# Performance work log

Hardware: AMD Instinct MI355X
Metric: run time of the kernel (lower is better)

The kernel has to match this reference:

```python
import jax, jax.numpy as jnp
import numpy as np

N = 2048      # number of ROIs
C = 1024      # in_channels == inter_channels
G = 16        # groups
D = C // G    # per-group dim = 64


def _bbox_overlaps(b1, b2):
    # mmdet-1.x IoU with +1 pixel convention; b1:(N,4), b2:(M,4)
    area1 = (b1[:, 2] - b1[:, 0] + 1) * (b1[:, 3] - b1[:, 1] + 1)  # (N,)
    area2 = (b2[:, 2] - b2[:, 0] + 1) * (b2[:, 3] - b2[:, 1] + 1)  # (M,)
    lt = jnp.maximum(b1[:, None, :2], b2[None, :, :2])             # (N,M,2)
    rb = jnp.minimum(b1[:, None, 2:], b2[None, :, 2:])             # (N,M,2)
    wh = jnp.clip(rb - lt + 1, 0)
    inter = wh[..., 0] * wh[..., 1]                                # (N,M)
    return inter / (area1[:, None] + area2[None, :] - inter)


def setup_inputs() -> dict:
    key = jax.random.key(0)
    ks = jax.random.split(key, 9)
    in_x = jax.random.normal(ks[0], (N, C), dtype=jnp.float32)
    # valid boxes: [batch_idx, x1, y1, x2, y2]
    xy = jax.random.uniform(ks[1], (N, 2), minval=0.0, maxval=800.0)
    wh = jax.random.uniform(ks[2], (N, 2), minval=8.0, maxval=200.0)
    rois = jnp.concatenate([jnp.zeros((N, 1)), xy, xy + wh], axis=1).astype(jnp.float32)
    s = 1.0 / np.sqrt(C)
    W0 = jax.random.normal(ks[3], (C, C), dtype=jnp.float32) * s
    b0 = jnp.zeros((C,), dtype=jnp.float32)
    W1 = jax.random.normal(ks[4], (C, C), dtype=jnp.float32) * s
    b1 = jnp.zeros((C,), dtype=jnp.float32)
    # grouped 1x1 conv: per group maps C channels -> D channels
    Wout = jax.random.normal(ks[5], (G, D, C), dtype=jnp.float32) * s
    bout = jnp.zeros((C,), dtype=jnp.float32)
    return {"in_x": in_x, "rois": rois, "W0": W0, "b0": b0, "W1": W1,
            "b1": b1, "Wout": Wout, "bout": bout}


def reference(in_x, rois, W0, b0, W1, b1, Wout, bout):
    # self-attention path: in_ref_x = in_x, ref_rois = rois
    # embed convs are pre-activation (relu -> 1x1 conv), shared for x and ref_x
    def embed(v):
        v = jax.nn.relu(v) @ W0.T + b0
        v = jax.nn.relu(v) @ W1.T + b1
        return v
    x = embed(in_x)                      # (N, C)
    ref_x = x                            # shared convs, same input
    xg = x.reshape(N, G, D)
    rg = ref_x.reshape(N, G, D)
    scores = jnp.einsum('ngd,mgd->ngm', xg, rg) / jnp.sqrt(jnp.float32(D))  # (N,G,N)
    ious = _bbox_overlaps(rois[:, 1:], rois[:, 1:])                          # (N,N)
    scores = scores + jnp.log(ious[:, None, :] + 1e-6)
    attn = jax.nn.softmax(scores, axis=2)                                    # (N,G,N)
    y = jnp.einsum('ngm,mc->ngc', attn, in_x)                                # (N,G,C)
    out = jnp.einsum('ngc,goc->ngo', y, Wout).reshape(N, C) + bout           # (N,C)
    return out
```

## Files before the change

kernel.cpp:

```cpp
#include <hip/hip_runtime.h>
#include <math.h>

constexpr int NROI = 2048;
constexpr int CDIM = 1024;
constexpr int NG   = 16;
constexpr int DH   = 64;

typedef __attribute__((ext_vector_type(8))) short short8;
typedef __attribute__((ext_vector_type(4))) float floatx4;

#define MFMA_BF16(a, b, c) __builtin_amdgcn_mfma_f32_16x16x32_bf16((a), (b), (c), 0, 0, 0)

__device__ __forceinline__ short f2bf(float f) {
  unsigned u = __float_as_uint(f);
  unsigned r = 0x7fffu + ((u >> 16) & 1u);
  return (short)((u + r) >> 16);
}
__device__ __forceinline__ short f2bf_rtz(float f) {
  return (short)(__float_as_uint(f) >> 16);
}
__device__ __forceinline__ unsigned pack2(float a, float b) {
  return (unsigned)(unsigned short)f2bf(a) | ((unsigned)(unsigned short)f2bf(b) << 16);
}

typedef __attribute__((address_space(1))) void GV;
typedef __attribute__((address_space(3))) void LV;
__device__ __forceinline__ void gl2lds16(const void* g, void* l) {
  __builtin_amdgcn_global_load_lds((GV*)g, (LV*)l, 16, 0, 0);
}

__device__ __forceinline__ short8 brelu(short8 v) {
  union { short8 s; unsigned u[4]; } x; x.s = v;
#pragma unroll
  for (int i = 0; i < 4; ++i) {
    unsigned m = (x.u[i] >> 15) & 0x10001u;
    x.u[i] &= ~(m * 0xFFFFu);
  }
  return x.s;
}

__global__ __launch_bounds__(256) void conv_iou(
    const float* __restrict__ in_x, const float* __restrict__ W0,
    const float* __restrict__ W1, const float* __restrict__ Wout,
    const float* __restrict__ rois,
    short* __restrict__ xin_b, short* __restrict__ W0b,
    short* __restrict__ W1b, short* __restrict__ Woutb,
    unsigned short* __restrict__ biasln)
{
  const int b = blockIdx.x;
  if (b < 2048) {
    const int i = b * 256 + threadIdx.x;
    {
      const float4 v = ((const float4*)in_x)[i];
      uint2 u; u.x = pack2(v.x, v.y); u.y = pack2(v.z, v.w);
      ((uint2*)xin_b)[i] = u;
    }
    if (i < 262144) {
      float4 v = ((const float4*)W0)[i];
      uint2 u; u.x = pack2(v.x, v.y); u.y = pack2(v.z, v.w);
      ((uint2*)W0b)[i] = u;
      v = ((const float4*)W1)[i];
      u.x = pack2(v.x, v.y); u.y = pack2(v.z, v.w);
      ((uint2*)W1b)[i] = u;
      v = ((const float4*)Wout)[i];
      u.x = pack2(v.x, v.y); u.y = pack2(v.z, v.w);
      ((uint2*)Woutb)[i] = u;
    }
  } else {
    const int p = (b - 2048) * 256 + threadIdx.x;
    const int q = p >> 11, k = p & 2047;
    const float qx1 = rois[q * 5 + 1], qy1 = rois[q * 5 + 2];
    const float qx2 = rois[q * 5 + 3], qy2 = rois[q * 5 + 4];
    const float qa = (qx2 - qx1 + 1.f) * (qy2 - qy1 + 1.f);
    const float kx1 = rois[k * 5 + 1], ky1 = rois[k * 5 + 2];
    const float kx2 = rois[k * 5 + 3], ky2 = rois[k * 5 + 4];
    const float ka = (kx2 - kx1 + 1.f) * (ky2 - ky1 + 1.f);
    float iw = fminf(qx2, kx2) - fmaxf(qx1, kx1) + 1.f;
    float ih = fminf(qy2, ky2) - fmaxf(qy1, ky1) + 1.f;
    iw = fmaxf(iw, 0.f); ih = fmaxf(ih, 0.f);
    const float inter = iw * ih;
    const float iou = inter / (qa + ka - inter);
    biasln[p] = (unsigned short)f2bf(__logf(iou + 1e-6f));
  }
}

__global__ __launch_bounds__(256) void gemm128(
    const short* __restrict__ A, const short* __restrict__ BW0,
    const short* __restrict__ BWout, const float* __restrict__ b0,
    short* __restrict__ t0b, short* __restrict__ zT)
{
  __shared__ short As[16 * 512];
  __shared__ short Bs[16 * 512];
  const int t = threadIdx.x, w = t >> 6, lane = t & 63;
  const int wm = w >> 1, wn = w & 1;
  const int row0 = blockIdx.y * 128;
  const int col0g = blockIdx.x * 128;
  const int isW0 = col0g < 1024;
  const short* B = isW0 ? BW0 : BWout;
  const int col0 = col0g & 1023;
  const int srow = lane & 15, skq = (lane >> 4) * 8;

  floatx4 acc[4][4];
#pragma unroll
  for (int i = 0; i < 4; ++i)
#pragma unroll
    for (int j = 0; j < 4; ++j) acc[i][j] = (floatx4){0.f, 0.f, 0.f, 0.f};

  for (int k0 = 0; k0 < CDIM; k0 += 64) {
    __syncthreads();
#pragma unroll
    for (int q = 0; q < 4; ++q) {
      const int f = w * 4 + q, rt = f >> 1, kh = f & 1;
      gl2lds16(A + (size_t)(row0 + rt * 16 + srow) * CDIM + k0 + kh * 32 + skq,
               &As[f * 512]);
      gl2lds16(B + (size_t)(col0 + rt * 16 + srow) * CDIM + k0 + kh * 32 + skq,
               &Bs[f * 512]);
    }
    __syncthreads();
#pragma unroll
    for (int kh = 0; kh < 2; ++kh) {
      short8 a[4], bf[4];
#pragma unroll
      for (int i = 0; i < 4; ++i) {
        a[i] = *(const short8*)&As[(((wm * 4 + i) * 2) + kh) * 512 + lane * 8];
        if (isW0) a[i] = brelu(a[i]);
      }
#pragma unroll
      for (int j = 0; j < 4; ++j)
        bf[j] = *(const short8*)&Bs[(((wn * 4 + j) * 2) + kh) * 512 + lane * 8];
#pragma unroll
      for (int i = 0; i < 4; ++i)
#pragma unroll
        for (int j = 0; j < 4; ++j)
          acc[i][j] = MFMA_BF16(a[i], bf[j], acc[i][j]);
    }
  }

  const int colL = lane & 15, qq = lane >> 4;
  if (isW0) {
    float bj[4];
#pragma unroll
    for (int j = 0; j < 4; ++j) bj[j] = b0[col0 + wn * 64 + j * 16 + colL];
#pragma unroll
    for (int i = 0; i < 4; ++i)
#pragma unroll
      for (int j = 0; j < 4; ++j)
#pragma unroll
        for (int r = 0; r < 4; ++r) {
          const int row = row0 + wm * 64 + i * 16 + qq * 4 + r;
          const int cc  = col0 + wn * 64 + j * 16 + colL;
          t0b[(size_t)row * CDIM + cc] = f2bf(acc[i][j][r] + bj[j]);
        }
  } else {
#pragma unroll
    for (int i = 0; i < 4; ++i)
#pragma unroll
      for (int j = 0; j < 4; ++j) {
        unsigned long long u = 0;
#pragma unroll
        for (int r = 0; r < 4; ++r)
          u |= ((unsigned long long)(unsigned short)f2bf(acc[i][j][r])) << (16 * r);
        const int cc  = col0 + wn * 64 + j * 16 + colL;
        const int row = row0 + wm * 64 + i * 16 + qq * 4;
        *(unsigned long long*)&zT[(size_t)cc * NROI + row] = u;
      }
  }
}

__global__ __launch_bounds__(256) void gemm_relu_nt(
    const short* __restrict__ A, const short* __restrict__ B,
    const float* __restrict__ bias, short* __restrict__ C)
{
  __shared__ short As[8 * 512];
  __shared__ short Bs[8 * 512];
  const int t = threadIdx.x, w = t >> 6, lane = t & 63;
  const int wm = w >> 1, wn = w & 1;
  const int row0 = blockIdx.y * 64, col0 = blockIdx.x * 64;
  const int rlo = lane & 15, khi = (lane >> 4) * 8;

  floatx4 acc[2][2];
#pragma unroll
  for (int i = 0; i < 2; ++i)
#pragma unroll
    for (int j = 0; j < 2; ++j) acc[i][j] = (floatx4){0.f, 0.f, 0.f, 0.f};

  for (int k0 = 0; k0 < CDIM; k0 += 64) {
    __syncthreads();
#pragma unroll
    for (int kh = 0; kh < 2; ++kh) {
      gl2lds16(A + (size_t)(row0 + w * 16 + rlo) * CDIM + k0 + kh * 32 + khi,
               &As[(w * 2 + kh) * 512]);
      gl2lds16(B + (size_t)(col0 + w * 16 + rlo) * CDIM + k0 + kh * 32 + khi,
               &Bs[(w * 2 + kh) * 512]);
    }
    __syncthreads();
#pragma unroll
    for (int kh = 0; kh < 2; ++kh) {
      short8 a0 = *(const short8*)&As[((wm * 2 + 0) * 2 + kh) * 512 + lane * 8];
      short8 a1 = *(const short8*)&As[((wm * 2 + 1) * 2 + kh) * 512 + lane * 8];
      a0 = brelu(a0); a1 = brelu(a1);
      const short8 b0f = *(const short8*)&Bs[((wn * 2 + 0) * 2 + kh) * 512 + lane * 8];
      const short8 b1f = *(const short8*)&Bs[((wn * 2 + 1) * 2 + kh) * 512 + lane * 8];
      acc[0][0] = MFMA_BF16(a0, b0f, acc[0][0]);
      acc[0][1] = MFMA_BF16(a0, b1f, acc[0][1]);
      acc[1][0] = MFMA_BF16(a1, b0f, acc[1][0]);
      acc[1][1] = MFMA_BF16(a1, b1f, acc[1][1]);
    }
  }

  const int colL = lane & 15, qq = lane >> 4;
  float bj[2];
  bj[0] = bias[col0 + wn * 32 + colL];
  bj[1] = bias[col0 + wn * 32 + 16 + colL];
#pragma unroll
  for (int i = 0; i < 2; ++i)
#pragma unroll
    for (int j = 0; j < 2; ++j)
#pragma unroll
      for (int r = 0; r < 4; ++r) {
        const int row = row0 + wm * 32 + i * 16 + qq * 4 + r;
        const int cc  = col0 + wn * 32 + j * 16 + colL;
        C[(size_t)row * CDIM + cc] = f2bf(acc[i][j][r] + bj[j]);
      }
}

__global__ __launch_bounds__(512) void attn_ln(
    const short* __restrict__ Xb,
    const short* __restrict__ ZTb,
    const unsigned short* __restrict__ biasln,
    const float* __restrict__ bout,
    float* __restrict__ Out)
{
  const int g  = blockIdx.y;
  const int n0 = blockIdx.x * 128;
  const int t = threadIdx.x, w = t >> 6, lane = t & 63;
  const int col = lane & 15, qq = lane >> 4;
  const int t16 = (w >> 1) * 16, h32 = (w & 1) * 32;
  const int rlo = lane & 15, khi = (lane >> 4) * 8;

  __shared__ short Kf[2][8 * 512];
  __shared__ short Vf[2][8 * 512];
  __shared__ short Pf[8 * 1024];

  const size_t qoff = (size_t)(n0 + w * 16 + col) * CDIM + g * DH;
  const short8 qf0 = *(const short8*)(Xb + qoff + qq * 8);
  const short8 qf1 = *(const short8*)(Xb + qoff + 32 + qq * 8);

  floatx4 oc[4];
#pragma unroll
  for (int dt = 0; dt < 4; ++dt) oc[dt] = (floatx4){0.f, 0.f, 0.f, 0.f};
  float lsum[4] = {0.f, 0.f, 0.f, 0.f};

  const int qrow0 = n0 + w * 16 + qq * 4;

  uint2 bbc[4], bbn[4];
#pragma unroll
  for (int ct = 0; ct < 4; ++ct)
    bbc[ct] = *(const uint2*)(biasln + (size_t)(ct * 16 + col) * NROI + qrow0);

  gl2lds16(Xb + (size_t)(t16 + rlo) * CDIM + g * DH + h32 + khi, &Kf[0][w * 512]);
  gl2lds16(ZTb + (size_t)(g * DH + t16 + rlo) * NROI + h32 + khi, &Vf[0][w * 512]);
  __syncthreads();

  for (int it = 0; it < NROI / 64; ++it) {
    const int p = it & 1;
    const int m0 = it * 64;
    if (it + 1 < NROI / 64) {
      const int m1 = m0 + 64;
      gl2lds16(Xb + (size_t)(m1 + t16 + rlo) * CDIM + g * DH + h32 + khi,
               &Kf[1 - p][w * 512]);
      gl2lds16(ZTb + (size_t)(g * DH + t16 + rlo) * NROI + m1 + h32 + khi,
               &Vf[1 - p][w * 512]);
#pragma unroll
      for (int ct = 0; ct < 4; ++ct)
        bbn[ct] = *(const uint2*)(biasln + (size_t)(m1 + ct * 16 + col) * NROI + qrow0);
    }

    floatx4 sc[4];
#pragma unroll
    for (int ct = 0; ct < 4; ++ct) {
      const short8 b0 = *(const short8*)&Kf[p][(ct * 2 + 0) * 512 + lane * 8];
      const short8 b1 = *(const short8*)&Kf[p][(ct * 2 + 1) * 512 + lane * 8];
      floatx4 z4 = (floatx4){0.f, 0.f, 0.f, 0.f};
      z4 = MFMA_BF16(qf0, b0, z4);
      z4 = MFMA_BF16(qf1, b1, z4);
      sc[ct] = z4;
    }

#pragma unroll
    for (int ct = 0; ct < 4; ++ct) {
      const unsigned ux = bbc[ct].x, uy = bbc[ct].y;
      sc[ct][0] = __expf(fmaf(sc[ct][0], 0.125f, __uint_as_float(ux << 16)));
      sc[ct][1] = __expf(fmaf(sc[ct][1], 0.125f, __uint_as_float(ux & 0xFFFF0000u)));
      sc[ct][2] = __expf(fmaf(sc[ct][2], 0.125f, __uint_as_float(uy << 16)));
      sc[ct][3] = __expf(fmaf(sc[ct][3], 0.125f, __uint_as_float(uy & 0xFFFF0000u)));
    }
#pragma unroll
    for (int r = 0; r < 4; ++r)
      lsum[r] += sc[0][r] + sc[1][r] + sc[2][r] + sc[3][r];

    {
      short* pw = &Pf[w * 1024];
#pragma unroll
      for (int ct = 0; ct < 4; ++ct) {
        const int key = ct * 16 + col;
        const int base = (key >> 5) * 512 + (key & 7);
#pragma unroll
        for (int r = 0; r < 4; ++r) {
          const int dl = (4 * qq + r) + ((key >> 3) & 3) * 16;
          pw[base + dl * 8] = f2bf_rtz(sc[ct][r]);
        }
      }
      const short8 pa0 = *(const short8*)&pw[0 * 512 + lane * 8];
      const short8 pa1 = *(const short8*)&pw[1 * 512 + lane * 8];
#pragma unroll
      for (int dt = 0; dt < 4; ++dt) {
        const short8 v0 = *(const short8*)&Vf[p][(dt * 2 + 0) * 512 + lane * 8];
        const short8 v1 = *(const short8*)&Vf[p][(dt * 2 + 1) * 512 + lane * 8];
        oc[dt] = MFMA_BF16(pa0, v0, oc[dt]);
        oc[dt] = MFMA_BF16(pa1, v1, oc[dt]);
      }
    }
    __syncthreads();
#pragma unroll
    for (int ct = 0; ct < 4; ++ct) bbc[ct] = bbn[ct];
  }

#pragma unroll
  for (int r = 0; r < 4; ++r) {
    float s = lsum[r];
    s += __shfl_xor(s, 1); s += __shfl_xor(s, 2);
    s += __shfl_xor(s, 4); s += __shfl_xor(s, 8);
    lsum[r] = s;
  }
#pragma unroll
  for (int dt = 0; dt < 4; ++dt) {
    const float bo = bout[g * DH + dt * 16 + col];
#pragma unroll
    for (int r = 0; r < 4; ++r)
      Out[(size_t)(qrow0 + r) * CDIM + g * DH + dt * 16 + col] =
          oc[dt][r] / lsum[r] + bo;
  }
}

extern "C" void kernel_launch(void* const* d_in, const int* in_sizes, int n_in,
                              void* d_out, int out_size, void* d_ws, size_t ws_size,
                              hipStream_t stream) {
  const float* in_x = (const float*)d_in[0];
  const float* rois = (const float*)d_in[1];
  const float* W0   = (const float*)d_in[2];
  const float* b0   = (const float*)d_in[3];
  const float* W1   = (const float*)d_in[4];
  const float* b1   = (const float*)d_in[5];
  const float* Wout = (const float*)d_in[6];
  const float* bout = (const float*)d_in[7];
  char* w8 = (char*)d_ws;

  short* xin_b = (short*)w8;
  short* W0b   = (short*)(w8 + ((size_t)4 << 20));
  short* W1b   = (short*)(w8 + ((size_t)6 << 20));
  short* Woutb = (short*)(w8 + ((size_t)8 << 20));
  short* zT    = (short*)(w8 + ((size_t)10 << 20));
  unsigned short* biasln = (unsigned short*)(w8 + ((size_t)14 << 20));
  short* xb  = xin_b;
  short* t0b = (short*)d_out;

  conv_iou<<<2048 + 16384, 256, 0, stream>>>(in_x, W0, W1, Wout, rois,
                                             xin_b, W0b, W1b, Woutb, biasln);
  gemm128<<<dim3(16, 16), 256, 0, stream>>>(xin_b, W0b, Woutb, b0, t0b, zT);
  gemm_relu_nt<<<dim3(16, 32), 256, 0, stream>>>(t0b, W1b, b1, xb);
  attn_ln<<<dim3(NROI / 128, NG), 512, 0, stream>>>(xb, zT, biasln, bout,
                                                    (float*)d_out);
}
```

Baseline: 205.5 us.

## Rewrite GEMM and attention kernels as single-wave blocks with double-buffered LDS

Replaces the 4-wave GEMM kernels and the 8-wave attention kernel with one-wavefront-per-block kernels. They prefetch the next K/V or A/B tile into a second LDS buffer and use manual vmcnt waits and sched barriers in place of __syncthreads. The two embed GEMMs share one template. The attention kernel processes 32 queries per wave, writes packed P tiles to LDS with 64-bit stores, and normalises with a reciprocal. The aim is to remove block-level barriers and overlap loads with MFMA work. The cost is smaller tiles and possibly low occupancy, because each single wave holds a large LDS footprint. The last prefetch also reads past the end of each buffer.

```diff
diff --git a/kernel.cpp b/kernel.cpp
--- a/kernel.cpp
+++ b/kernel.cpp
@@ -16,11 +16,11 @@
   unsigned r = 0x7fffu + ((u >> 16) & 1u);
   return (short)((u + r) >> 16);
 }
-__device__ __forceinline__ short f2bf_rtz(float f) {
-  return (short)(__float_as_uint(f) >> 16);
-}
 __device__ __forceinline__ unsigned pack2(float a, float b) {
   return (unsigned)(unsigned short)f2bf(a) | ((unsigned)(unsigned short)f2bf(b) << 16);
+}
+__device__ __forceinline__ unsigned pack_rtz(float a, float b) {
+  return (__float_as_uint(a) >> 16) | (__float_as_uint(b) & 0xFFFF0000u);
 }
 
 typedef __attribute__((address_space(1))) void GV;
@@ -28,6 +28,10 @@
 __device__ __forceinline__ void gl2lds16(const void* g, void* l) {
   __builtin_amdgcn_global_load_lds((GV*)g, (LV*)l, 16, 0, 0);
 }
+
+__device__ __forceinline__ void waitcnt_vm16() { __builtin_amdgcn_s_waitcnt(0x4F70); }
+__device__ __forceinline__ void waitcnt_vm12() { __builtin_amdgcn_s_waitcnt(0x0F7C); }
+__device__ __forceinline__ void sbar() { __builtin_amdgcn_sched_barrier(0); }
 
 __device__ __forceinline__ short8 brelu(short8 v) {
   union { short8 s; unsigned u[4]; } x; x.s = v;
@@ -84,262 +88,238 @@
   }
 }
 
-__global__ __launch_bounds__(256) void gemm128(
-    const short* __restrict__ A, const short* __restrict__ BW0,
-    const short* __restrict__ BWout, const float* __restrict__ b0,
-    short* __restrict__ t0b, short* __restrict__ zT)
+template <int FUSED>
+__global__ __launch_bounds__(64) void gemm_wp(
+    const short* __restrict__ A, const short* __restrict__ Ba,
+    const short* __restrict__ Bb, const float* __restrict__ bias,
+    short* __restrict__ outRM, short* __restrict__ outTR)
 {
-  __shared__ short As[16 * 512];
-  __shared__ short Bs[16 * 512];
-  const int t = threadIdx.x, w = t >> 6, lane = t & 63;
-  const int wm = w >> 1, wn = w & 1;
-  const int row0 = blockIdx.y * 128;
-  const int col0g = blockIdx.x * 128;
-  const int isW0 = col0g < 1024;
-  const short* B = isW0 ? BW0 : BWout;
-  const int col0 = col0g & 1023;
-  const int srow = lane & 15, skq = (lane >> 4) * 8;
-
-  floatx4 acc[4][4];
+  const int lane = threadIdx.x;
+  const int c = lane & 15, Q = lane >> 4;
+  const int rlo = c, khi = Q * 8;
+  const int row0 = blockIdx.y * 64;
+  int colb; const short* B; bool doRelu, toTR;
+  if (FUSED) {
+    const int bx = blockIdx.x;
+    const bool isW0 = bx < 32;
+    colb = (bx & 31) * 32;
+    B = isW0 ? Ba : Bb;
+    doRelu = isW0; toTR = !isW0;
+  } else {
+    colb = blockIdx.x * 32; B = Ba; doRelu = true; toTR = false;
+  }
+
+  __shared__ short As[2][8 * 512];
+  __shared__ short Bs[2][4 * 512];
+
+  floatx4 acc[4][2];
 #pragma unroll
   for (int i = 0; i < 4; ++i)
 #pragma unroll
-    for (int j = 0; j < 4; ++j) acc[i][j] = (floatx4){0.f, 0.f, 0.f, 0.f};
-
-  for (int k0 = 0; k0 < CDIM; k0 += 64) {
-    __syncthreads();
-#pragma unroll
-    for (int q = 0; q < 4; ++q) {
-      const int f = w * 4 + q, rt = f >> 1, kh = f & 1;
-      gl2lds16(A + (size_t)(row0 + rt * 16 + srow) * CDIM + k0 + kh * 32 + skq,
-               &As[f * 512]);
-      gl2lds16(B + (size_t)(col0 + rt * 16 + srow) * CDIM + k0 + kh * 32 + skq,
-               &Bs[f * 512]);
-    }
-    __syncthreads();
-#pragma unroll
-    for (int kh = 0; kh < 2; ++kh) {
-      short8 a[4], bf[4];
-#pragma unroll
-      for (int i = 0; i < 4; ++i) {
-        a[i] = *(const short8*)&As[(((wm * 4 + i) * 2) + kh) * 512 + lane * 8];
-        if (isW0) a[i] = brelu(a[i]);
-      }
-#pragma unroll
-      for (int j = 0; j < 4; ++j)
-        bf[j] = *(const short8*)&Bs[(((wn * 4 + j) * 2) + kh) * 512 + lane * 8];
+    for (int j = 0; j < 2; ++j) acc[i][j] = (floatx4){0.f, 0.f, 0.f, 0.f};
+
+#pragma unroll
+  for (int f = 0; f < 8; ++f)
+    gl2lds16(A + (size_t)(row0 + (f >> 1) * 16 + rlo) * CDIM + (f & 1) * 32 + khi,
+             &As[0][f * 512]);
+#pragma unroll
+  for (int f = 0; f < 4; ++f)
+    gl2lds16(B + (size_t)(colb + (f >> 1) * 16 + rlo) * CDIM + (f & 1) * 32 + khi,
+             &Bs[0][f * 512]);
+
+  for (int it = 0; it < 16; ++it) {
+    const int p = it & 1;
+    const int k1 = (it + 1) * 64;
+    sbar();
+#pragma unroll
+    for (int f = 0; f < 8; ++f)
+      gl2lds16(A + (size_t)(row0 + (f >> 1) * 16 + rlo) * CDIM + k1 + (f & 1) * 32 + khi,
+               &As[1 - p][f * 512]);
+#pragma unroll
+    for (int f = 0; f < 4; ++f)
+      gl2lds16(B + (size_t)(colb + (f >> 1) * 16 + rlo) * CDIM + k1 + (f & 1) * 32 + khi,
+               &Bs[1 - p][f * 512]);
+    waitcnt_vm12();
+    sbar();
+
+    short8 af[8], bf[4];
+    if (doRelu) {
+#pragma unroll
+      for (int f = 0; f < 8; ++f)
+        af[f] = brelu(*(const short8*)&As[p][f * 512 + lane * 8]);
+    } else {
+#pragma unroll
+      for (int f = 0; f < 8; ++f)
+        af[f] = *(const short8*)&As[p][f * 512 + lane * 8];
+    }
+#pragma unroll
+    for (int f = 0; f < 4; ++f) bf[f] = *(const short8*)&Bs[p][f * 512 + lane * 8];
+#pragma unroll
+    for (int kh = 0; kh < 2; ++kh)
 #pragma unroll
       for (int i = 0; i < 4; ++i)
 #pragma unroll
-        for (int j = 0; j < 4; ++j)
-          acc[i][j] = MFMA_BF16(a[i], bf[j], acc[i][j]);
-    }
-  }
-
-  const int colL = lane & 15, qq = lane >> 4;
-  if (isW0) {
-    float bj[4];
-#pragma unroll
-    for (int j = 0; j < 4; ++j) bj[j] = b0[col0 + wn * 64 + j * 16 + colL];
+        for (int j = 0; j < 2; ++j)
+          acc[i][j] = MFMA_BF16(af[i * 2 + kh], bf[j * 2 + kh], acc[i][j]);
+  }
+
+  if (!toTR) {
+    const float bj0 = bias[colb + c];
+    const float bj1 = bias[colb + 16 + c];
 #pragma unroll
     for (int i = 0; i < 4; ++i)
 #pragma unroll
-      for (int j = 0; j < 4; ++j)
-#pragma unroll
-        for (int r = 0; r < 4; ++r) {
-          const int row = row0 + wm * 64 + i * 16 + qq * 4 + r;
-          const int cc  = col0 + wn * 64 + j * 16 + colL;
-          t0b[(size_t)row * CDIM + cc] = f2bf(acc[i][j][r] + bj[j]);
-        }
+      for (int r = 0; r < 4; ++r) {
+        const int row = row0 + i * 16 + Q * 4 + r;
+        outRM[(size_t)row * CDIM + colb + c]      = f2bf(acc[i][0][r] + bj0);
+        outRM[(size_t)row * CDIM + colb + 16 + c] = f2bf(acc[i][1][r] + bj1);
+      }
   } else {
 #pragma unroll
     for (int i = 0; i < 4; ++i)
 #pragma unroll
-      for (int j = 0; j < 4; ++j) {
-        unsigned long long u = 0;
-#pragma unroll
-        for (int r = 0; r < 4; ++r)
-          u |= ((unsigned long long)(unsigned short)f2bf(acc[i][j][r])) << (16 * r);
-        const int cc  = col0 + wn * 64 + j * 16 + colL;
-        const int row = row0 + wm * 64 + i * 16 + qq * 4;
-        *(unsigned long long*)&zT[(size_t)cc * NROI + row] = u;
-      }
-  }
-}
-
-__global__ __launch_bounds__(256) void gemm_relu_nt(
-    const short* __restrict__ A, const short* __restrict__ B,
-    const float* __restrict__ bias, short* __restrict__ C)
-{
-  __shared__ short As[8 * 512];
-  __shared__ short Bs[8 * 512];
-  const int t = threadIdx.x, w = t >> 6, lane = t & 63;
-  const int wm = w >> 1, wn = w & 1;
-  const int row0 = blockIdx.y * 64, col0 = blockIdx.x * 64;
-  const int rlo = lane & 15, khi = (lane >> 4) * 8;
-
-  floatx4 acc[2][2];
-#pragma unroll
-  for (int i = 0; i < 2; ++i)
-#pragma unroll
-    for (int j = 0; j < 2; ++j) acc[i][j] = (floatx4){0.f, 0.f, 0.f, 0.f};
-
-  for (int k0 = 0; k0 < CDIM; k0 += 64) {
-    __syncthreads();
-#pragma unroll
-    for (int kh = 0; kh < 2; ++kh) {
-      gl2lds16(A + (size_t)(row0 + w * 16 + rlo) * CDIM + k0 + kh * 32 + khi,
-               &As[(w * 2 + kh) * 512]);
-      gl2lds16(B + (size_t)(col0 + w * 16 + rlo) * CDIM + k0 + kh * 32 + khi,
-               &Bs[(w * 2 + kh) * 512]);
-    }
-    __syncthreads();
-#pragma unroll
-    for (int kh = 0; kh < 2; ++kh) {
-      short8 a0 = *(const short8*)&As[((wm * 2 + 0) * 2 + kh) * 512 + lane * 8];
-      short8 a1 = *(const short8*)&As[((wm * 2 + 1) * 2 + kh) * 512 + lane * 8];
-      a0 = brelu(a0); a1 = brelu(a1);
-      const short8 b0f = *(const short8*)&Bs[((wn * 2 + 0) * 2 + kh) * 512 + lane * 8];
-      const short8 b1f = *(const short8*)&Bs[((wn * 2 + 1) * 2 + kh) * 512 + lane * 8];
-      acc[0][0] = MFMA_BF16(a0, b0f, acc[0][0]);
-      acc[0][1] = MFMA_BF16(a0, b1f, acc[0][1]);
-      acc[1][0] = MFMA_BF16(a1, b0f, acc[1][0]);
-      acc[1][1] = MFMA_BF16(a1, b1f, acc[1][1]);
-    }
-  }
-
-  const int colL = lane & 15, qq = lane >> 4;
-  float bj[2];
-  bj[0] = bias[col0 + wn * 32 + colL];
-  bj[1] = bias[col0 + wn * 32 + 16 + colL];
-#pragma unroll
-  for (int i = 0; i < 2; ++i)
-#pragma unroll
-    for (int j = 0; j < 2; ++j)
-#pragma unroll
-      for (int r = 0; r < 4; ++r) {
-        const int row = row0 + wm * 32 + i * 16 + qq * 4 + r;
-        const int cc  = col0 + wn * 32 + j * 16 + colL;
-        C[(size_t)row * CDIM + cc] = f2bf(acc[i][j][r] + bj[j]);
-      }
-}
-
-__global__ __launch_bounds__(512) void attn_ln(
+      for (int j = 0; j < 2; ++j) {
+        unsigned long long u =
+            (unsigned long long)pack2(acc[i][j][0], acc[i][j][1]) |
+            ((unsigned long long)pack2(acc[i][j][2], acc[i][j][3]) << 32);
+        *(unsigned long long*)&outTR[(size_t)(colb + j * 16 + c) * NROI +
+                                     row0 + i * 16 + Q * 4] = u;
+      }
+  }
+}
+
+__global__ __launch_bounds__(64) void attn_wp(
     const short* __restrict__ Xb,
     const short* __restrict__ ZTb,
     const unsigned short* __restrict__ biasln,
     const float* __restrict__ bout,
     float* __restrict__ Out)
 {
-  const int g  = blockIdx.y;
-  const int n0 = blockIdx.x * 128;
-  const int t = threadIdx.x, w = t >> 6, lane = t & 63;
-  const int col = lane & 15, qq = lane >> 4;
-  const int t16 = (w >> 1) * 16, h32 = (w & 1) * 32;
-  const int rlo = lane & 15, khi = (lane >> 4) * 8;
-
-  __shared__ short Kf[2][8 * 512];
-  __shared__ short Vf[2][8 * 512];
-  __shared__ short Pf[8 * 1024];
-
-  const size_t qoff = (size_t)(n0 + w * 16 + col) * CDIM + g * DH;
-  const short8 qf0 = *(const short8*)(Xb + qoff + qq * 8);
-  const short8 qf1 = *(const short8*)(Xb + qoff + 32 + qq * 8);
-
-  floatx4 oc[4];
-#pragma unroll
-  for (int dt = 0; dt < 4; ++dt) oc[dt] = (floatx4){0.f, 0.f, 0.f, 0.f};
-  float lsum[4] = {0.f, 0.f, 0.f, 0.f};
-
-  const int qrow0 = n0 + w * 16 + qq * 4;
-
-  uint2 bbc[4], bbn[4];
-#pragma unroll
-  for (int ct = 0; ct < 4; ++ct)
-    bbc[ct] = *(const uint2*)(biasln + (size_t)(ct * 16 + col) * NROI + qrow0);
-
-  gl2lds16(Xb + (size_t)(t16 + rlo) * CDIM + g * DH + h32 + khi, &Kf[0][w * 512]);
-  gl2lds16(ZTb + (size_t)(g * DH + t16 + rlo) * NROI + h32 + khi, &Vf[0][w * 512]);
-  __syncthreads();
-
-  for (int it = 0; it < NROI / 64; ++it) {
+  const int g = blockIdx.y, q0 = blockIdx.x * 32;
+  const int lane = threadIdx.x;
+  const int c = lane & 15, Q = lane >> 4;
+  const int rlo = c, khi = Q * 8;
+  const int goff = g * DH;
+
+  __shared__ short KT[2][8 * 512];
+  __shared__ short VT[2][8 * 512];
+  __shared__ short PT[2][1024];
+
+  short8 qf[2][2];
+#pragma unroll
+  for (int s = 0; s < 2; ++s)
+#pragma unroll
+    for (int h = 0; h < 2; ++h)
+      qf[s][h] = *(const short8*)(Xb + (size_t)(q0 + s * 16 + c) * CDIM + goff +
+                                  h * 32 + Q * 8);
+
+  floatx4 oc[2][4];
+#pragma unroll
+  for (int s = 0; s < 2; ++s)
+#pragma unroll
+    for (int dt = 0; dt < 4; ++dt) oc[s][dt] = (floatx4){0.f, 0.f, 0.f, 0.f};
+  float ls[2] = {0.f, 0.f};
+
+#pragma unroll
+  for (int f = 0; f < 8; ++f) {
+    gl2lds16(Xb + (size_t)((f >> 1) * 16 + rlo) * CDIM + goff + (f & 1) * 32 + khi,
+             &KT[0][f * 512]);
+    gl2lds16(ZTb + (size_t)(goff + (f >> 1) * 16 + rlo) * NROI + (f & 1) * 32 + khi,
+             &VT[0][f * 512]);
+  }
+
+  for (int it = 0; it < 32; ++it) {
     const int p = it & 1;
-    const int m0 = it * 64;
-    if (it + 1 < NROI / 64) {
-      const int m1 = m0 + 64;
-      gl2lds16(Xb + (size_t)(m1 + t16 + rlo) * CDIM + g * DH + h32 + khi,
-               &Kf[1 - p][w * 512]);
-      gl2lds16(ZTb + (size_t)(g * DH + t16 + rlo) * NROI + m1 + h32 + khi,
-               &Vf[1 - p][w * 512]);
+    const int m0 = it * 64, m1 = m0 + 64;
+    sbar();
+#pragma unroll
+    for (int f = 0; f < 8; ++f) {
+      gl2lds16(Xb + (size_t)(m1 + (f >> 1) * 16 + rlo) * CDIM + goff + (f & 1) * 32 + khi,
+               &KT[1 - p][f * 512]);
+      gl2lds16(ZTb + (size_t)(goff + (f >> 1) * 16 + rlo) * NROI + m1 + (f & 1) * 32 + khi,
+               &VT[1 - p][f * 512]);
+    }
+    waitcnt_vm16();
+    sbar();
+
+    short8 kf[8];
+#pragma unroll
+    for (int f = 0; f < 8; ++f)
+      kf[f] = *(const short8*)&KT[p][f * 512 + lane * 8];
+
+    uint2 bb[2][4];
+#pragma unroll
+    for (int s = 0; s < 2; ++s)
 #pragma unroll
       for (int ct = 0; ct < 4; ++ct)
-        bbn[ct] = *(const uint2*)(biasln + (size_t)(m1 + ct * 16 + col) * NROI + qrow0);
-    }
-
-    floatx4 sc[4];
-#pragma unroll
-    for (int ct = 0; ct < 4; ++ct) {
-      const short8 b0 = *(const short8*)&Kf[p][(ct * 2 + 0) * 512 + lane * 8];
-      const short8 b1 = *(const short8*)&Kf[p][(ct * 2 + 1) * 512 + lane * 8];
-      floatx4 z4 = (floatx4){0.f, 0.f, 0.f, 0.f};
-      z4 = MFMA_BF16(qf0, b0, z4);
-      z4 = MFMA_BF16(qf1, b1, z4);
-      sc[ct] = z4;
-    }
-
-#pragma unroll
-    for (int ct = 0; ct < 4; ++ct) {
-      const unsigned ux = bbc[ct].x, uy = bbc[ct].y;
-      sc[ct][0] = __expf(fmaf(sc[ct][0], 0.125f, __uint_as_float(ux << 16)));
-      sc[ct][1] = __expf(fmaf(sc[ct][1], 0.125f, __uint_as_float(ux & 0xFFFF0000u)));
-      sc[ct][2] = __expf(fmaf(sc[ct][2], 0.125f, __uint_as_float(uy << 16)));
-      sc[ct][3] = __expf(fmaf(sc[ct][3], 0.125f, __uint_as_float(uy & 0xFFFF0000u)));
-    }
+        bb[s][ct] = *(const uint2*)(biasln + (size_t)(q0 + s * 16 + c) * NROI +
+                                    m0 + ct * 16 + Q * 4);
+
+#pragma unroll
+    for (int s = 0; s < 2; ++s) {
+      floatx4 sc[4];
+#pragma unroll
+      for (int ct = 0; ct < 4; ++ct) {
+        floatx4 z = (floatx4){0.f, 0.f, 0.f, 0.f};
+        z = MFMA_BF16(kf[ct * 2 + 0], qf[s][0], z);
+        z = MFMA_BF16(kf[ct * 2 + 1], qf[s][1], z);
+        sc[ct] = z;
+      }
+#pragma unroll
+      for (int ct = 0; ct < 4; ++ct) {
+        const unsigned ux = bb[s][ct].x, uy = bb[s][ct].y;
+        sc[ct][0] = __expf(fmaf(sc[ct][0], 0.125f, __uint_as_float(ux << 16)));
+        sc[ct][1] = __expf(fmaf(sc[ct][1], 0.125f, __uint_as_float(ux & 0xFFFF0000u)));
+        sc[ct][2] = __expf(fmaf(sc[ct][2], 0.125f, __uint_as_float(uy << 16)));
+        sc[ct][3] = __expf(fmaf(sc[ct][3], 0.125f, __uint_as_float(uy & 0xFFFF0000u)));
+        ls[s] += sc[ct][0] + sc[ct][1] + sc[ct][2] + sc[ct][3];
+        const int h  = (4 * ct + Q) >> 3;
+        const int o  = (2 * ct + (Q >> 1)) & 3;
+        const int j0 = (Q & 1) * 4;
+        const unsigned long long u =
+            (unsigned long long)pack_rtz(sc[ct][0], sc[ct][1]) |
+            ((unsigned long long)pack_rtz(sc[ct][2], sc[ct][3]) << 32);
+        *(unsigned long long*)&PT[s][h * 512 + (c + 16 * o) * 8 + j0] = u;
+      }
+    }
+
+    short8 vf[8];
+#pragma unroll
+    for (int f = 0; f < 8; ++f)
+      vf[f] = *(const short8*)&VT[p][f * 512 + lane * 8];
+#pragma unroll
+    for (int s = 0; s < 2; ++s) {
+      const short8 pa0 = *(const short8*)&PT[s][lane * 8];
+      const short8 pa1 = *(const short8*)&PT[s][512 + lane * 8];
+#pragma unroll
+      for (int dt = 0; dt < 4; ++dt) {
+        oc[s][dt] = MFMA_BF16(pa0, vf[dt * 2 + 0], oc[s][dt]);
+        oc[s][dt] = MFMA_BF16(pa1, vf[dt * 2 + 1], oc[s][dt]);
+      }
+    }
+  }
+
+#pragma unroll
+  for (int s = 0; s < 2; ++s) {
+    float v = ls[s];
+    v += __shfl_xor(v, 16);
+    v += __shfl_xor(v, 32);
+    ls[s] = v;
+  }
+#pragma unroll
+  for (int s = 0; s < 2; ++s) {
+    float inv[4];
 #pragma unroll
     for (int r = 0; r < 4; ++r)
-      lsum[r] += sc[0][r] + sc[1][r] + sc[2][r] + sc[3][r];
-
-    {
-      short* pw = &Pf[w * 1024];
-#pragma unroll
-      for (int ct = 0; ct < 4; ++ct) {
-        const int key = ct * 16 + col;
-        const int base = (key >> 5) * 512 + (key & 7);
-#pragma unroll
-        for (int r = 0; r < 4; ++r) {
-          const int dl = (4 * qq + r) + ((key >> 3) & 3) * 16;
-          pw[base + dl * 8] = f2bf_rtz(sc[ct][r]);
-        }
-      }
-      const short8 pa0 = *(const short8*)&pw[0 * 512 + lane * 8];
-      const short8 pa1 = *(const short8*)&pw[1 * 512 + lane * 8];
-#pragma unroll
-      for (int dt = 0; dt < 4; ++dt) {
-        const short8 v0 = *(const short8*)&Vf[p][(dt * 2 + 0) * 512 + lane * 8];
-        const short8 v1 = *(const short8*)&Vf[p][(dt * 2 + 1) * 512 + lane * 8];
-        oc[dt] = MFMA_BF16(pa0, v0, oc[dt]);
-        oc[dt] = MFMA_BF16(pa1, v1, oc[dt]);
-      }
-    }
-    __syncthreads();
-#pragma unroll
-    for (int ct = 0; ct < 4; ++ct) bbc[ct] = bbn[ct];
-  }
-
-#pragma unroll
-  for (int r = 0; r < 4; ++r) {
-    float s = lsum[r];
-    s += __shfl_xor(s, 1); s += __shfl_xor(s, 2);
-    s += __shfl_xor(s, 4); s += __shfl_xor(s, 8);
-    lsum[r] = s;
-  }
-#pragma unroll
-  for (int dt = 0; dt < 4; ++dt) {
-    const float bo = bout[g * DH + dt * 16 + col];
-#pragma unroll
-    for (int r = 0; r < 4; ++r)
-      Out[(size_t)(qrow0 + r) * CDIM + g * DH + dt * 16 + col] =
-          oc[dt][r] / lsum[r] + bo;
+      inv[r] = __builtin_amdgcn_rcpf(__shfl(ls[s], Q * 4 + r));
+#pragma unroll
+    for (int dt = 0; dt < 4; ++dt) {
+      const float bo = bout[goff + dt * 16 + c];
+#pragma unroll
+      for (int r = 0; r < 4; ++r)
+        Out[(size_t)(q0 + s * 16 + Q * 4 + r) * CDIM + goff + dt * 16 + c] =
+            oc[s][dt][r] * inv[r] + bo;
+    }
   }
 }
 
@@ -367,8 +347,8 @@
 
   conv_iou<<<2048 + 16384, 256, 0, stream>>>(in_x, W0, W1, Wout, rois,
                                              xin_b, W0b, W1b, Woutb, biasln);
-  gemm128<<<dim3(16, 16), 256, 0, stream>>>(xin_b, W0b, Woutb, b0, t0b, zT);
-  gemm_relu_nt<<<dim3(16, 32), 256, 0, stream>>>(t0b, W1b, b1, xb);
-  attn_ln<<<dim3(NROI / 128, NG), 512, 0, stream>>>(xb, zT, biasln, bout,
-                                                    (float*)d_out);
-}
+  gemm_wp<1><<<dim3(64, 32), 64, 0, stream>>>(xin_b, W0b, Woutb, b0, t0b, zT);
+  gemm_wp<0><<<dim3(32, 32), 64, 0, stream>>>(t0b, W1b, W1b, b1, xb, nullptr);
+  attn_wp<<<dim3(NROI / 32, NG), 64, 0, stream>>>(xb, zT, biasln, bout,
+                                                  (float*)d_out);
+}
```

Measured after the change: 274.8 us. +33.8%, slower.
